# Optimization experiments

Hardware: AMD Instinct MI355X
Metric: run time of the kernel (lower is better)

The kernel has to match this reference:

```python
import jax, jax.numpy as jnp
import numpy as np

IMAGE_SIZE = 320
SIGMA = 0.01      # soft-edge width in NDC units (~1.6 px at 320 res)
CHUNK = 128       # faces per scan step (bounds peak memory)


def setup_inputs() -> dict:
    key = jax.random.key(0)
    k1, k2 = jax.random.split(key)
    verts = jax.random.normal(k1, (4, 778, 3), dtype=jnp.float32) * 0.5
    faces = jax.random.randint(k2, (1538, 3), 0, 778, dtype=jnp.int32)
    return {"verts": verts, "faces": faces}


def _silhouette(verts, faces):
    B = verts.shape[0]
    S = IMAGE_SIZE
    # NMR.forward flips the y axis of verts before rendering
    v = verts * jnp.array([1.0, -1.0, 1.0], dtype=verts.dtype)
    xy = v[..., :2]  # orthographic projection (perspective=False)
    F = faces.shape[0]
    n_chunks = -(-F // CHUNK)
    Fp = n_chunks * CHUNK
    faces_p = jnp.pad(faces, ((0, Fp - F), (0, 0)))
    valid = (jnp.arange(Fp) < F).astype(verts.dtype)
    tri = xy[:, faces_p]  # [B, Fp, 3, 2]
    tri = jnp.moveaxis(tri.reshape(B, n_chunks, CHUNK, 3, 2), 1, 0)  # [nc,B,C,3,2]
    valid = valid.reshape(n_chunks, CHUNK)
    # pixel centers in NDC [-1, 1]
    lin = (jnp.arange(S, dtype=verts.dtype) + 0.5) / S * 2.0 - 1.0
    py, px = jnp.meshgrid(lin, lin, indexing="ij")
    px = px.reshape(-1)  # [P]
    py = py.reshape(-1)

    def edge_d(a, b, sgn):
        # signed distance of every pixel to oriented edge a->b: [B, C, P]
        ex = b[..., 0] - a[..., 0]
        ey = b[..., 1] - a[..., 1]
        inv_len = 1.0 / (jnp.sqrt(ex * ex + ey * ey) + 1e-8)
        d = (ex[..., None] * (py[None, None, :] - a[..., 1:2])
             - ey[..., None] * (px[None, None, :] - a[..., 0:1]))
        return sgn[..., None] * d * inv_len[..., None]

    def body(acc, chunk):
        tri_c, m = chunk  # [B,C,3,2], [C]
        v0, v1, v2 = tri_c[..., 0, :], tri_c[..., 1, :], tri_c[..., 2, :]
        # orientation sign so CW / CCW triangles are handled uniformly
        area2 = ((v1[..., 0] - v0[..., 0]) * (v2[..., 1] - v0[..., 1])
                 - (v1[..., 1] - v0[..., 1]) * (v2[..., 0] - v0[..., 0]))
        sgn = jnp.sign(area2)
        logp = (jax.nn.log_sigmoid(edge_d(v0, v1, sgn) / SIGMA)
                + jax.nn.log_sigmoid(edge_d(v1, v2, sgn) / SIGMA)
                + jax.nn.log_sigmoid(edge_d(v2, v0, sgn) / SIGMA))
        prob = jnp.clip(jnp.exp(logp) * m[None, :, None], 0.0, 1.0 - 1e-6)
        return acc + jnp.sum(jnp.log1p(-prob), axis=1), None

    acc0 = jnp.zeros((B, S * S), dtype=verts.dtype)
    acc, _ = jax.lax.scan(body, acc0, (tri, valid))
    # silhouette = 1 - prod_f (1 - coverage_f), accumulated in log space
    return (1.0 - jnp.exp(acc)).reshape(B, S, S)


def reference(verts, faces):
    return _silhouette(verts, faces)
```

## Files before the change

### kernel.cpp

```cpp
#include <hip/hip_runtime.h>
#include <math.h>


#define IMG_S 320
#define N_TILES 40
#define N_FACES 1538
#define N_VERTS 778
#define N_BATCH 4
#define FP 1600
#define TILE 8
#define MAXB 256
#define MAXCAND 1544
#define NWAVE 4
#define INV_SIGMA 100.0f
#define T_CUT 12.0f
#define ACC_CUT_P 2.2603294e-6f
#define LOG2_1EM6 -19.9315686f

__global__ __launch_bounds__(256)
void prep_faces(const float* __restrict__ verts,
                const int* __restrict__ faces,
                float4* __restrict__ gE0,
                float4* __restrict__ gE1,
                float4* __restrict__ gE2,
                unsigned int* __restrict__ gBB)
{
    const int f = blockIdx.x * 256 + threadIdx.x;
    const int b = blockIdx.z;
    if (f >= N_FACES) return;

    const float* vb = verts + (size_t)b * N_VERTS * 3;
    const int i0 = faces[f * 3 + 0];
    const int i1 = faces[f * 3 + 1];
    const int i2 = faces[f * 3 + 2];
    const float x0 = vb[i0 * 3 + 0], y0 = -vb[i0 * 3 + 1];
    const float x1 = vb[i1 * 3 + 0], y1 = -vb[i1 * 3 + 1];
    const float x2 = vb[i2 * 3 + 0], y2 = -vb[i2 * 3 + 1];

    const float dx1 = x1 - x0, dy1 = y1 - y0;
    const float dx2 = x2 - x0, dy2 = y2 - y0;
    const float area2 = __builtin_fmaf(dx1, dy2, -__fmul_rn(dy1, dx2));
    const float sgn = (area2 > 0.0f) ? 1.0f : ((area2 < 0.0f) ? -1.0f : 0.0f);

    const size_t o = (size_t)b * FP + f;
    float4 e0, e1, e2;
    {
        const float ex = x1 - x0, ey = y1 - y0;
        const float s = sgn * INV_SIGMA / (sqrtf(ex * ex + ey * ey) + 1e-8f);
        e0 = make_float4(-s * ey, s * ex, s * (ey * x0 - ex * y0), 0.0f);
    }
    {
        const float ex = x2 - x1, ey = y2 - y1;
        const float s = sgn * INV_SIGMA / (sqrtf(ex * ex + ey * ey) + 1e-8f);
        e1 = make_float4(-s * ey, s * ex, s * (ey * x1 - ex * y1), 0.0f);
    }
    {
        const float ex = x0 - x2, ey = y0 - y2;
        const float s = sgn * INV_SIGMA / (sqrtf(ex * ex + ey * ey) + 1e-8f);
        e2 = make_float4(-s * ey, s * ex, s * (ey * x2 - ex * y2), 0.0f);
    }
    gE0[o] = e0;
    gE1[o] = e1;
    gE2[o] = e2;

    const float pw = 2.0f / IMG_S;
    const float rr = 3.5f * pw;
    const float r0 = rr * (fabsf(e0.x) + fabsf(e0.y));
    const float r1 = rr * (fabsf(e1.x) + fabsf(e1.y));
    const float r2 = rr * (fabsf(e2.x) + fabsf(e2.y));
    const float C0 = e0.z + T_CUT + r0 + 0.5f;
    const float C1 = e1.z + T_CUT + r1 + 0.5f;
    const float C2 = e2.z + T_CUT + r2 + 0.5f;

    float xmn = 1e30f, xmx = -1e30f, ymn = 1e30f, ymx = -1e30f;
    bool ok = true;
    {
        const float ww = e0.x * e1.y - e0.y * e1.x;
        if (fabsf(ww) < 1e-3f) ok = false;
        else {
            const float iw = 1.0f / ww;
            const float x = (e0.y * C1 - C0 * e1.y) * iw;
            const float y = (C0 * e1.x - e0.x * C1) * iw;
            xmn = fminf(xmn, x); xmx = fmaxf(xmx, x);
            ymn = fminf(ymn, y); ymx = fmaxf(ymx, y);
        }
    }
    {
        const float ww = e1.x * e2.y - e1.y * e2.x;
        if (fabsf(ww) < 1e-3f) ok = false;
        else {
            const float iw = 1.0f / ww;
            const float x = (e1.y * C2 - C1 * e2.y) * iw;
            const float y = (C1 * e2.x - e1.x * C2) * iw;
            xmn = fminf(xmn, x); xmx = fmaxf(xmx, x);
            ymn = fminf(ymn, y); ymx = fmaxf(ymx, y);
        }
    }
    {
        const float ww = e2.x * e0.y - e2.y * e0.x;
        if (fabsf(ww) < 1e-3f) ok = false;
        else {
            const float iw = 1.0f / ww;
            const float x = (e2.y * C0 - C2 * e0.y) * iw;
            const float y = (C2 * e0.x - e2.x * C0) * iw;
            xmn = fminf(xmn, x); xmx = fmaxf(xmx, x);
            ymn = fminf(ymn, y); ymx = fmaxf(ymx, y);
        }
    }
    if (!ok || !(xmn <= xmx) || !(ymn <= ymx)) {
        xmn = -1.0f; xmx = 1.0f; ymn = -1.0f; ymx = 1.0f;
    }
    xmn = fmaxf(xmn, -1.0f); xmx = fminf(xmx, 1.0f);
    ymn = fmaxf(ymn, -1.0f); ymx = fminf(ymx, 1.0f);

    const int tx0 = max(0,  (int)floorf(((xmn + 1.0f) * 160.0f - 4.0f) * 0.125f) - 1);
    const int tx1 = min(N_TILES - 1, (int)ceilf(((xmx + 1.0f) * 160.0f - 4.0f) * 0.125f) + 1);
    const int ty0 = max(0,  (int)floorf(((ymn + 1.0f) * 160.0f - 4.0f) * 0.125f) - 1);
    const int ty1 = min(N_TILES - 1, (int)ceilf(((ymx + 1.0f) * 160.0f - 4.0f) * 0.125f) + 1);

    gBB[o] = (unsigned)tx0 | ((unsigned)max(tx1, tx0) << 8) |
             ((unsigned)ty0 << 16) | ((unsigned)max(ty1, ty0) << 24);
}

__global__ __launch_bounds__(256)
void silhouette_ws(const float4* __restrict__ gE0,
                   const float4* __restrict__ gE1,
                   const float4* __restrict__ gE2,
                   const unsigned int* __restrict__ gBB,
                   float* __restrict__ out)
{
    __shared__ float4 sE0[MAXB];
    __shared__ float4 sE1[MAXB];
    __shared__ float4 sE2[MAXB];
    __shared__ unsigned short sCand[MAXCAND];
    __shared__ float sAcc[256];
    __shared__ int sNC;
    __shared__ int sCount;
    __shared__ int sAlive;
    __shared__ int sCover;

    const int t    = threadIdx.x;
    const int wave = t >> 6;
    const int lane = t & 63;
    const int p    = t & 63;
    const int plx  = p & 7;
    const int ply  = p >> 3;
    const int b    = blockIdx.z;
    const int tx   = blockIdx.x;
    const int ty   = blockIdx.y;
    const int gx   = tx * TILE + plx;
    const int gy   = ty * TILE + ply;

    const float w  = 2.0f / IMG_S;
    const float px = (gx + 0.5f) * w - 1.0f;
    const float py = (gy + 0.5f) * w - 1.0f;
    const float cx = (tx * TILE + 4) * w - 1.0f;
    const float cy = (ty * TILE + 4) * w - 1.0f;
    const float rr = 3.5f * w;

    const float4* gb0 = gE0 + (size_t)b * FP;
    const float4* gb1 = gE1 + (size_t)b * FP;
    const float4* gb2 = gE2 + (size_t)b * FP;
    const unsigned int* bbb = gBB + (size_t)b * FP;

    if (t == 0) sNC = 0;
    __syncthreads();
    for (int fb = 0; fb < N_FACES; fb += 256) {
        const int f = fb + t;
        bool hit = false;
        if (f < N_FACES) {
            const unsigned bb = bbb[f];
            hit = (tx >= (int)(bb & 255u))         && (tx <= (int)((bb >> 8) & 255u)) &&
                  (ty >= (int)((bb >> 16) & 255u)) && (ty <= (int)(bb >> 24));
        }
        const unsigned long long mh = __ballot(hit);
        int wb = 0;
        if (lane == 0) {
            const int nw = __popcll(mh);
            if (nw) wb = atomicAdd(&sNC, nw);
        }
        wb = __shfl(wb, 0);
        if (hit) sCand[wb + __popcll(mh & ((1ull << lane) - 1ull))] =
                     (unsigned short)f;
    }
    __syncthreads();
    const int nCand = sNC;

    float acc = 1.0f;

    for (int base = 0; base < nCand; base += MAXB) {
        const int nn2 = min(MAXB, nCand - base);

        sAcc[t] = acc;
        if (t == 0) { sCount = 0; sAlive = 0; sCover = 0; }
        __syncthreads();
        const float tot = sAcc[p] * sAcc[p + 64] * sAcc[p + 128] * sAcc[p + 192];
        const bool alive = (tot > ACC_CUT_P);
        if (alive) sAlive = 1;
        __syncthreads();
        if (sAlive == 0) break;

        {
            const int k = base + t;
            const bool vald = (k < nCand);
            const int fc = sCand[vald ? k : base];
            const float4 e0 = gb0[fc];
            const float4 e1 = gb1[fc];
            const float4 e2 = gb2[fc];
            const float c0 = fmaf(e0.x, cx, fmaf(e0.y, cy, e0.z));
            const float c1 = fmaf(e1.x, cx, fmaf(e1.y, cy, e1.z));
            const float c2 = fmaf(e2.x, cx, fmaf(e2.y, cy, e2.z));
            const float r0 = rr * (fabsf(e0.x) + fabsf(e0.y));
            const float r1 = rr * (fabsf(e1.x) + fabsf(e1.y));
            const float r2 = rr * (fabsf(e2.x) + fabsf(e2.y));
            const float m_hi = fminf(c0 + r0, fminf(c1 + r1, c2 + r2));
            const float m_lo = fminf(c0 - r0, fminf(c1 - r1, c2 - r2));
            const bool isCov  = vald && (m_lo > T_CUT);
            const bool isBand = vald && !isCov && (m_hi > -T_CUT);

            const unsigned long long mb = __ballot(isBand);
            int wbase = 0;
            if (lane == 0) {
                const int nw = __popcll(mb);
                if (nw) wbase = atomicAdd(&sCount, nw);
            }
            wbase = __shfl(wbase, 0);
            if (isBand) {
                const int pos = wbase + __popcll(mb & ((1ull << lane) - 1ull));
                sE0[pos] = e0;
                sE1[pos] = e1;
                sE2[pos] = e2;
            }
            const unsigned long long mc = __ballot(isCov);
            if (lane == 0) {
                const int ncv = __popcll(mc);
                if (ncv) atomicAdd(&sCover, ncv);
            }
            (void)nn2;
        }
        __syncthreads();

        const float coverF = exp2f((float)sCover * LOG2_1EM6);
        bool live = alive && (acc * coverF > ACC_CUT_P);
        if (wave == 0) acc *= coverF;

        const int n = sCount;
        int j = wave;
        while (j < n) {
            if (__ballot(live) == 0ull) break;
            const int j1 = j + NWAVE;
            const int j1c = (j1 < n) ? j1 : j;
            const float4 A0 = sE0[j],   A1 = sE1[j],   A2 = sE2[j];
            const float4 B0 = sE0[j1c], B1 = sE1[j1c], B2 = sE2[j1c];
            {
                const float xa = fmaf(A0.x, px, fmaf(A0.y, py, A0.z));
                const float xb = fmaf(A1.x, px, fmaf(A1.y, py, A1.z));
                const float xc = fmaf(A2.x, px, fmaf(A2.y, py, A2.z));
                const float m = fminf(xa, fminf(xb, xc));
                if (live && m > -T_CUT) {
                    const float da = 1.0f + __expf(-xa);
                    const float db = 1.0f + __expf(-xb);
                    const float dc = 1.0f + __expf(-xc);
                    const float f = fmaxf(
                        1.0f - __builtin_amdgcn_rcpf(da * db * dc), 1e-6f);
                    acc *= f;
                    live = (acc > ACC_CUT_P);
                }
            }
            if (j1 < n) {
                const float xa = fmaf(B0.x, px, fmaf(B0.y, py, B0.z));
                const float xb = fmaf(B1.x, px, fmaf(B1.y, py, B1.z));
                const float xc = fmaf(B2.x, px, fmaf(B2.y, py, B2.z));
                const float m = fminf(xa, fminf(xb, xc));
                if (live && m > -T_CUT) {
                    const float da = 1.0f + __expf(-xa);
                    const float db = 1.0f + __expf(-xb);
                    const float dc = 1.0f + __expf(-xc);
                    const float f = fmaxf(
                        1.0f - __builtin_amdgcn_rcpf(da * db * dc), 1e-6f);
                    acc *= f;
                    live = (acc > ACC_CUT_P);
                }
            }
            j += 2 * NWAVE;
        }
    }

    sAcc[t] = acc;
    __syncthreads();
    if (t < 64) {
        const float tot = sAcc[p] * sAcc[p + 64] * sAcc[p + 128] * sAcc[p + 192];
        out[(size_t)b * (IMG_S * IMG_S) + (size_t)gy * IMG_S + gx] = 1.0f - tot;
    }
}

extern "C" void kernel_launch(void* const* d_in, const int* in_sizes, int n_in,
                              void* d_out, int out_size, void* d_ws, size_t ws_size,
                              hipStream_t stream) {
    const float* verts = (const float*)d_in[0];
    const int* faces = (const int*)d_in[1];
    float* out = (float*)d_out;

    float4* gE0 = (float4*)d_ws;
    float4* gE1 = gE0 + (size_t)N_BATCH * FP;
    float4* gE2 = gE1 + (size_t)N_BATCH * FP;
    unsigned int* gBB = (unsigned int*)(gE2 + (size_t)N_BATCH * FP);

    dim3 pgrid((N_FACES + 255) / 256, 1, N_BATCH);
    prep_faces<<<pgrid, 256, 0, stream>>>(verts, faces, gE0, gE1, gE2, gBB);

    dim3 grid(IMG_S / TILE, IMG_S / TILE, N_BATCH);
    silhouette_ws<<<grid, 256, 0, stream>>>(gE0, gE1, gE2, gBB, out);
}
```

Before: 85.95 us.

## Fuse bbox candidate compaction into chunked face classification loop

Removes the separate pass that compacted bounding-box-hit face indices into a shared candidate list. Faces are now scanned directly in four fixed chunks of 384, with the bbox test, edge-plane loads and cover/band classification done in a single pass per chunk. This drops one barrier-separated phase and the indirect index lookup. In exchange every block loads edge data for all faces rather than only the bbox hits, and the early-exit check now runs per fixed chunk instead of per candidate batch.

Result: faster. 83.49 us (-2.9%).

```diff
diff --git a/kernel.cpp b/kernel.cpp
--- a/kernel.cpp
+++ b/kernel.cpp
@@ -9,8 +9,9 @@
 #define N_BATCH 4
 #define FP 1600
 #define TILE 8
-#define MAXB 256
-#define MAXCAND 1544
+#define CHUNK_F 384
+#define N_CHUNKS 4
+#define MAXB 388
 #define NWAVE 4
 #define INV_SIGMA 100.0f
 #define T_CUT 12.0f
@@ -132,9 +133,7 @@
     __shared__ float4 sE0[MAXB];
     __shared__ float4 sE1[MAXB];
     __shared__ float4 sE2[MAXB];
-    __shared__ unsigned short sCand[MAXCAND];
     __shared__ float sAcc[256];
-    __shared__ int sNC;
     __shared__ int sCount;
     __shared__ int sAlive;
     __shared__ int sCover;
@@ -163,50 +162,34 @@
     const float4* gb2 = gE2 + (size_t)b * FP;
     const unsigned int* bbb = gBB + (size_t)b * FP;
 
-    if (t == 0) sNC = 0;
-    __syncthreads();
-    for (int fb = 0; fb < N_FACES; fb += 256) {
-        const int f = fb + t;
-        bool hit = false;
-        if (f < N_FACES) {
-            const unsigned bb = bbb[f];
-            hit = (tx >= (int)(bb & 255u))         && (tx <= (int)((bb >> 8) & 255u)) &&
-                  (ty >= (int)((bb >> 16) & 255u)) && (ty <= (int)(bb >> 24));
-        }
-        const unsigned long long mh = __ballot(hit);
-        int wb = 0;
-        if (lane == 0) {
-            const int nw = __popcll(mh);
-            if (nw) wb = atomicAdd(&sNC, nw);
-        }
-        wb = __shfl(wb, 0);
-        if (hit) sCand[wb + __popcll(mh & ((1ull << lane) - 1ull))] =
-                     (unsigned short)f;
-    }
-    __syncthreads();
-    const int nCand = sNC;
-
     float acc = 1.0f;
 
-    for (int base = 0; base < nCand; base += MAXB) {
-        const int nn2 = min(MAXB, nCand - base);
+    for (int c = 0; c < N_CHUNKS; ++c) {
+        const int base = c * CHUNK_F;
+        const int end  = (c == N_CHUNKS - 1) ? N_FACES : base + CHUNK_F;
 
         sAcc[t] = acc;
         if (t == 0) { sCount = 0; sAlive = 0; sCover = 0; }
         __syncthreads();
+
         const float tot = sAcc[p] * sAcc[p + 64] * sAcc[p + 128] * sAcc[p + 192];
         const bool alive = (tot > ACC_CUT_P);
         if (alive) sAlive = 1;
         __syncthreads();
+
         if (sAlive == 0) break;
 
-        {
-            const int k = base + t;
-            const bool vald = (k < nCand);
-            const int fc = sCand[vald ? k : base];
-            const float4 e0 = gb0[fc];
-            const float4 e1 = gb1[fc];
-            const float4 e2 = gb2[fc];
+        for (int fb = base; fb < end; fb += 256) {
+            const int fc = fb + t;
+            const bool vald = (fc < end);
+            const int fcc = vald ? fc : (end - 1);
+            const float4 e0 = gb0[fcc];
+            const float4 e1 = gb1[fcc];
+            const float4 e2 = gb2[fcc];
+            const unsigned bb = bbb[fcc];
+            const bool hit =
+                (tx >= (int)(bb & 255u))         && (tx <= (int)((bb >> 8) & 255u)) &&
+                (ty >= (int)((bb >> 16) & 255u)) && (ty <= (int)(bb >> 24));
             const float c0 = fmaf(e0.x, cx, fmaf(e0.y, cy, e0.z));
             const float c1 = fmaf(e1.x, cx, fmaf(e1.y, cy, e1.z));
             const float c2 = fmaf(e2.x, cx, fmaf(e2.y, cy, e2.z));
@@ -215,8 +198,8 @@
             const float r2 = rr * (fabsf(e2.x) + fabsf(e2.y));
             const float m_hi = fminf(c0 + r0, fminf(c1 + r1, c2 + r2));
             const float m_lo = fminf(c0 - r0, fminf(c1 - r1, c2 - r2));
-            const bool isCov  = vald && (m_lo > T_CUT);
-            const bool isBand = vald && !isCov && (m_hi > -T_CUT);
+            const bool isCov  = vald && hit && (m_lo > T_CUT);
+            const bool isBand = vald && hit && !isCov && (m_hi > -T_CUT);
 
             const unsigned long long mb = __ballot(isBand);
             int wbase = 0;
@@ -236,7 +219,6 @@
                 const int ncv = __popcll(mc);
                 if (ncv) atomicAdd(&sCover, ncv);
             }
-            (void)nn2;
         }
         __syncthreads();
 
```
